# Performance work log

Hardware: AMD Instinct MI355X
Metric: run time of the kernel (lower is better)

The kernel has to match this reference:

```python
import jax, jax.numpy as jnp
import numpy as np

TEMPERATURE = 0.5
EPS = 1e-8  # matches torch cosine_similarity eps guard semantics (norm clamp)


def setup_inputs() -> dict:
    key = jax.random.key(0)
    k1, k2 = jax.random.split(key)
    B, D = 4096, 256
    z_i = jax.random.normal(k1, (B, D), dtype=jnp.float32)
    z_j = jax.random.normal(k2, (B, D), dtype=jnp.float32)
    return {"z_i": z_i, "z_j": z_j}


def reference(z_i, z_j):
    B = z_i.shape[0]
    z = jnp.concatenate([z_i, z_j], axis=0)            # [2B, D]
    # cosine similarity: normalize once, then GEMM
    norm = jnp.maximum(jnp.linalg.norm(z, axis=1, keepdims=True), EPS)
    zn = z / norm                                       # [2B, D]
    sim = zn @ zn.T                                     # [2B, 2B]
    # positives: diag(sim, +B) and diag(sim, -B)
    idx = jnp.arange(B)
    sim_ij = sim[idx, idx + B]
    sim_ji = sim[idx + B, idx]
    positives = jnp.concatenate([sim_ij, sim_ji])       # [2B]
    # masked denominator: exclude self-similarity
    mask = 1.0 - jnp.eye(2 * B, dtype=sim.dtype)
    denom = jnp.sum(mask * jnp.exp(sim / TEMPERATURE), axis=1)  # [2B]
    all_losses = -jnp.log(jnp.exp(positives / TEMPERATURE) / denom)
    return jnp.sum(all_losses) / (2 * B)
```

## Files before the change

kernel.cpp:

```cpp
#include <hip/hip_runtime.h>
#include <hip/hip_bf16.h>
#include <cstdint>
#include <cstddef>
#include <math.h>

#define D 256
#define TEMP_INV 2.0f
#define EPS_NORM 1e-8f
#define NTILES 2080
#define GRID 512

typedef __attribute__((ext_vector_type(8))) short bf16x8;
typedef __attribute__((ext_vector_type(4))) float f32x4;

__global__ void __launch_bounds__(256) normalize_rows(
    const float* __restrict__ zi, const float* __restrict__ zj,
    __hip_bfloat16* __restrict__ zn, float* __restrict__ denom, int B) {
  int row = blockIdx.x * 4 + (threadIdx.x >> 6);
  int lane = threadIdx.x & 63;
  if (threadIdx.x < 4) denom[blockIdx.x * 4 + threadIdx.x] = 0.0f;
  const float* src = (row < B) ? (zi + (size_t)row * D)
                               : (zj + (size_t)(row - B) * D);
  float4 v = ((const float4*)src)[lane];
  float ss = v.x * v.x + v.y * v.y + v.z * v.z + v.w * v.w;
  for (int off = 32; off; off >>= 1) ss += __shfl_xor(ss, off);
  float rn = 1.0f / fmaxf(sqrtf(ss), EPS_NORM);
  union { ushort4 u; __hip_bfloat16 h[4]; } o;
  o.h[0] = __float2bfloat16(v.x * rn);
  o.h[1] = __float2bfloat16(v.y * rn);
  o.h[2] = __float2bfloat16(v.z * rn);
  o.h[3] = __float2bfloat16(v.w * rn);
  ((ushort4*)zn)[(size_t)row * (D / 4) + lane] = o.u;
}

__device__ __forceinline__ void load_lds_16B(const __hip_bfloat16* g,
                                             __hip_bfloat16* l) {
  __builtin_amdgcn_global_load_lds(
      (const __attribute__((address_space(1))) void*)g,
      (__attribute__((address_space(3))) void*)l, 16, 0, 0);
}

__device__ __forceinline__ void decode_tile(int t, int Nb, int& by, int& bx) {
  float fb = (2.0f * Nb + 1.0f -
              sqrtf((float)((2 * Nb + 1) * (2 * Nb + 1) - 8 * t))) * 0.5f;
  int y = (int)fb;
  while ((y + 1) * Nb - ((y + 1) * y) / 2 <= t) ++y;
  while (y * Nb - (y * (y - 1)) / 2 > t) --y;
  by = y;
  bx = y + (t - (y * Nb - (y * (y - 1)) / 2));
}

__device__ __forceinline__ void stage_tile(
    const __hip_bfloat16* __restrict__ zn,
    __hip_bfloat16* Ash, __hip_bfloat16* Bsh,
    int bm, int bn, int k0, int wrow0, int lane) {
  const int lr4 = lane >> 4;
  const int lc16 = lane & 15;
#pragma unroll
  for (int s = 0; s < 8; ++s) {
    int r = wrow0 + s * 4 + lr4;
    int chunk = lc16 ^ (r & 7);
    const __hip_bfloat16* ga = zn + (size_t)(bm + r) * D + k0 + chunk * 8;
    const __hip_bfloat16* gb = zn + (size_t)(bn + r) * D + k0 + chunk * 8;
    load_lds_16B(ga, &Ash[(wrow0 + s * 4) * 128]);
    load_lds_16B(gb, &Bsh[(wrow0 + s * 4) * 128]);
  }
}

__device__ __forceinline__ void compute_k128(
    const __hip_bfloat16* Ash, const __hip_bfloat16* Bsh,
    f32x4 acc[4][4], int wy, int wx, int frow, int quad) {
  const int f7 = frow & 7;
#pragma unroll
  for (int kk = 0; kk < 4; ++kk) {
    bf16x8 a[4], b[4];
#pragma unroll
    for (int i = 0; i < 4; ++i)
      a[i] = *(const bf16x8*)
          &Ash[(wy * 64 + i * 16 + frow) * 128 + (((kk * 4 + quad) ^ f7)) * 8];
#pragma unroll
    for (int j = 0; j < 4; ++j)
      b[j] = *(const bf16x8*)
          &Bsh[(wx * 64 + j * 16 + frow) * 128 + (((kk * 4 + quad) ^ f7)) * 8];
#pragma unroll
    for (int i = 0; i < 4; ++i)
#pragma unroll
      for (int j = 0; j < 4; ++j)
        acc[i][j] =
            __builtin_amdgcn_mfma_f32_16x16x32_bf16(a[i], b[j], acc[i][j], 0, 0, 0);
  }
}

__global__ void __launch_bounds__(256) ntxent_gemm(
    const __hip_bfloat16* __restrict__ zn,
    float* __restrict__ denom, float* __restrict__ pos, int B) {
  __shared__ __align__(16) __hip_bfloat16 Ash[128 * 128];
  __shared__ __align__(16) __hip_bfloat16 Bsh[128 * 128];

  const int Nb = (2 * B) / 128;
  const int tid = threadIdx.x;
  const int wid = tid >> 6;
  const int lane = tid & 63;
  const int wy = wid >> 1, wx = wid & 1;
  const int wrow0 = wid * 32;
  const int frow = lane & 15;
  const int quad = lane >> 4;
  const int colq = lane & 15;

  int t = blockIdx.x;
  int by, bx;
  decode_tile(t, Nb, by, bx);
  int bm = by * 128, bn = bx * 128;
  stage_tile(zn, Ash, Bsh, bm, bn, 0, wrow0, lane);

  while (true) {
    f32x4 acc[4][4] = {};
    __syncthreads();
    compute_k128(Ash, Bsh, acc, wy, wx, frow, quad);
    __syncthreads();
    stage_tile(zn, Ash, Bsh, bm, bn, 128, wrow0, lane);
    __syncthreads();
    compute_k128(Ash, Bsh, acc, wy, wx, frow, quad);
    __syncthreads();

    int nt = t + GRID;
    bool more = (nt < NTILES);
    int nbm = 0, nbn = 0;
    if (more) {
      int nby, nbx;
      decode_tile(nt, Nb, nby, nbx);
      nbm = nby * 128;
      nbn = nbx * 128;
      stage_tile(zn, Ash, Bsh, nbm, nbn, 0, wrow0, lane);
    }

    const bool isDiag = (bm == bn);
    const bool isPos = (bn == bm + B);
    float cs[4] = {0.0f, 0.0f, 0.0f, 0.0f};
#pragma unroll
    for (int i = 0; i < 4; ++i) {
#pragma unroll
      for (int r = 0; r < 4; ++r) {
        int row = bm + wy * 64 + i * 16 + quad * 4 + r;
        float rs = 0.0f;
#pragma unroll
        for (int j = 0; j < 4; ++j) {
          int col = bn + wx * 64 + j * 16 + colq;
          float v = acc[i][j][r];
          float e = __expf(v * TEMP_INV);
          e = (isDiag && col == row) ? 0.0f : e;
          rs += e;
          cs[j] += e;
          if (isPos && col == row + B) { pos[row] = v; pos[col] = v; }
        }
        rs += __shfl_xor(rs, 1);
        rs += __shfl_xor(rs, 2);
        rs += __shfl_xor(rs, 4);
        rs += __shfl_xor(rs, 8);
        if (colq == 0) atomicAdd(&denom[row], rs);
      }
    }
    if (!isDiag) {
#pragma unroll
      for (int j = 0; j < 4; ++j) {
        float c = cs[j];
        c += __shfl_xor(c, 16);
        c += __shfl_xor(c, 32);
        if (quad == 0) atomicAdd(&denom[bn + wx * 64 + j * 16 + colq], c);
      }
    }
    if (!more) break;
    t = nt;
    bm = nbm;
    bn = nbn;
  }
}

__global__ void __launch_bounds__(1024) finalize(
    const float* __restrict__ denom, const float* __restrict__ pos,
    float* __restrict__ out, int N) {
  __shared__ float red[16];
  const int tid = threadIdx.x;
  float s = 0.0f;
  for (int i = tid; i < N / 4; i += 1024) {
    float4 d = ((const float4*)denom)[i];
    float4 p = ((const float4*)pos)[i];
    s += __logf(d.x) - p.x * TEMP_INV;
    s += __logf(d.y) - p.y * TEMP_INV;
    s += __logf(d.z) - p.z * TEMP_INV;
    s += __logf(d.w) - p.w * TEMP_INV;
  }
  for (int off = 32; off; off >>= 1) s += __shfl_xor(s, off);
  if ((tid & 63) == 0) red[tid >> 6] = s;
  __syncthreads();
  if (tid < 16) {
    s = red[tid];
    s += __shfl_xor(s, 1);
    s += __shfl_xor(s, 2);
    s += __shfl_xor(s, 4);
    s += __shfl_xor(s, 8);
    if (tid == 0) out[0] = s / (float)N;
  }
}

extern "C" void kernel_launch(void* const* d_in, const int* in_sizes, int n_in,
                              void* d_out, int out_size, void* d_ws, size_t ws_size,
                              hipStream_t stream) {
  const float* zi = (const float*)d_in[0];
  const float* zj = (const float*)d_in[1];
  const int B = in_sizes[0] / D;
  const int N = 2 * B;

  __hip_bfloat16* zn = (__hip_bfloat16*)d_ws;
  float* denom = (float*)((char*)d_ws + (size_t)N * D * sizeof(__hip_bfloat16));
  float* pos = denom + N;

  normalize_rows<<<N / 4, 256, 0, stream>>>(zi, zj, zn, denom, B);
  ntxent_gemm<<<GRID, 256, 0, stream>>>(zn, denom, pos, B);
  finalize<<<1, 1024, 0, stream>>>(denom, pos, (float*)d_out, N);
}
```

Measured before the change: 122.8 us.

## Launch one block per tile with K=64 register-prefetched LDS staging

Replaces the persistent 512-block loop with a launch of one block per upper-triangular tile (2080 blocks). The K loop is split into four 64-wide steps. The next step's global loads go into registers while MFMAs run on the current LDS buffer, replacing the direct global-to-LDS loads. LDS per block is halved and launch bounds request 3 waves per SIMD to raise occupancy, at the cost of more block launches and extra VGPR pressure from the prefetch registers.

```diff
diff --git a/kernel.cpp b/kernel.cpp
--- a/kernel.cpp
+++ b/kernel.cpp
@@ -8,7 +8,6 @@
 #define TEMP_INV 2.0f
 #define EPS_NORM 1e-8f
 #define NTILES 2080
-#define GRID 512
 
 typedef __attribute__((ext_vector_type(8))) short bf16x8;
 typedef __attribute__((ext_vector_type(4))) float f32x4;
@@ -33,13 +32,6 @@
   ((ushort4*)zn)[(size_t)row * (D / 4) + lane] = o.u;
 }
 
-__device__ __forceinline__ void load_lds_16B(const __hip_bfloat16* g,
-                                             __hip_bfloat16* l) {
-  __builtin_amdgcn_global_load_lds(
-      (const __attribute__((address_space(1))) void*)g,
-      (__attribute__((address_space(3))) void*)l, 16, 0, 0);
-}
-
 __device__ __forceinline__ void decode_tile(int t, int Nb, int& by, int& bx) {
   float fb = (2.0f * Nb + 1.0f -
               sqrtf((float)((2 * Nb + 1) * (2 * Nb + 1) - 8 * t))) * 0.5f;
@@ -50,129 +42,116 @@
   bx = y + (t - (y * Nb - (y * (y - 1)) / 2));
 }
 
-__device__ __forceinline__ void stage_tile(
-    const __hip_bfloat16* __restrict__ zn,
-    __hip_bfloat16* Ash, __hip_bfloat16* Bsh,
-    int bm, int bn, int k0, int wrow0, int lane) {
-  const int lr4 = lane >> 4;
-  const int lc16 = lane & 15;
-#pragma unroll
-  for (int s = 0; s < 8; ++s) {
-    int r = wrow0 + s * 4 + lr4;
-    int chunk = lc16 ^ (r & 7);
-    const __hip_bfloat16* ga = zn + (size_t)(bm + r) * D + k0 + chunk * 8;
-    const __hip_bfloat16* gb = zn + (size_t)(bn + r) * D + k0 + chunk * 8;
-    load_lds_16B(ga, &Ash[(wrow0 + s * 4) * 128]);
-    load_lds_16B(gb, &Bsh[(wrow0 + s * 4) * 128]);
-  }
-}
-
-__device__ __forceinline__ void compute_k128(
-    const __hip_bfloat16* Ash, const __hip_bfloat16* Bsh,
-    f32x4 acc[4][4], int wy, int wx, int frow, int quad) {
-  const int f7 = frow & 7;
-#pragma unroll
-  for (int kk = 0; kk < 4; ++kk) {
-    bf16x8 a[4], b[4];
-#pragma unroll
-    for (int i = 0; i < 4; ++i)
-      a[i] = *(const bf16x8*)
-          &Ash[(wy * 64 + i * 16 + frow) * 128 + (((kk * 4 + quad) ^ f7)) * 8];
-#pragma unroll
-    for (int j = 0; j < 4; ++j)
-      b[j] = *(const bf16x8*)
-          &Bsh[(wx * 64 + j * 16 + frow) * 128 + (((kk * 4 + quad) ^ f7)) * 8];
-#pragma unroll
-    for (int i = 0; i < 4; ++i)
-#pragma unroll
-      for (int j = 0; j < 4; ++j)
-        acc[i][j] =
-            __builtin_amdgcn_mfma_f32_16x16x32_bf16(a[i], b[j], acc[i][j], 0, 0, 0);
-  }
-}
-
-__global__ void __launch_bounds__(256) ntxent_gemm(
+__global__ void __launch_bounds__(256, 3) ntxent_gemm(
     const __hip_bfloat16* __restrict__ zn,
     float* __restrict__ denom, float* __restrict__ pos, int B) {
-  __shared__ __align__(16) __hip_bfloat16 Ash[128 * 128];
-  __shared__ __align__(16) __hip_bfloat16 Bsh[128 * 128];
+  __shared__ __align__(16) __hip_bfloat16 Ash[128 * 64];
+  __shared__ __align__(16) __hip_bfloat16 Bsh[128 * 64];
 
   const int Nb = (2 * B) / 128;
+  int by, bx;
+  decode_tile(blockIdx.x, Nb, by, bx);
+  const int bm = by * 128;
+  const int bn = bx * 128;
+  const bool isDiag = (by == bx);
+  const bool isPos = (bx == by + B / 128);
+
   const int tid = threadIdx.x;
   const int wid = tid >> 6;
   const int lane = tid & 63;
   const int wy = wid >> 1, wx = wid & 1;
   const int wrow0 = wid * 32;
+
+  const int r8 = lane >> 3;
+  const int c8 = lane & 7;
+
   const int frow = lane & 15;
   const int quad = lane >> 4;
+  const int f7 = frow & 7;
+
+  f32x4 acc[4][4] = {};
+  float4 va[4], vb[4];
+
+#pragma unroll
+  for (int s = 0; s < 4; ++s) {
+    int r = wrow0 + s * 8 + r8;
+    va[s] = *(const float4*)(zn + (size_t)(bm + r) * D + c8 * 8);
+    vb[s] = *(const float4*)(zn + (size_t)(bn + r) * D + c8 * 8);
+  }
+
+#pragma unroll
+  for (int k0i = 0; k0i < 4; ++k0i) {
+    __syncthreads();
+#pragma unroll
+    for (int s = 0; s < 4; ++s) {
+      int r = wrow0 + s * 8 + r8;
+      int swz = c8 ^ (r & 7);
+      *(float4*)&Ash[r * 64 + swz * 8] = va[s];
+      *(float4*)&Bsh[r * 64 + swz * 8] = vb[s];
+    }
+    __syncthreads();
+    if (k0i < 3) {
+      const int k0n = (k0i + 1) * 64;
+#pragma unroll
+      for (int s = 0; s < 4; ++s) {
+        int r = wrow0 + s * 8 + r8;
+        va[s] = *(const float4*)(zn + (size_t)(bm + r) * D + k0n + c8 * 8);
+        vb[s] = *(const float4*)(zn + (size_t)(bn + r) * D + k0n + c8 * 8);
+      }
+    }
+#pragma unroll
+    for (int kk = 0; kk < 2; ++kk) {
+      bf16x8 a[4], b[4];
+#pragma unroll
+      for (int i = 0; i < 4; ++i)
+        a[i] = *(const bf16x8*)
+            &Ash[(wy * 64 + i * 16 + frow) * 64 + ((kk * 4 + quad) ^ f7) * 8];
+#pragma unroll
+      for (int j = 0; j < 4; ++j)
+        b[j] = *(const bf16x8*)
+            &Bsh[(wx * 64 + j * 16 + frow) * 64 + ((kk * 4 + quad) ^ f7) * 8];
+#pragma unroll
+      for (int i = 0; i < 4; ++i)
+#pragma unroll
+        for (int j = 0; j < 4; ++j)
+          acc[i][j] =
+              __builtin_amdgcn_mfma_f32_16x16x32_bf16(a[i], b[j], acc[i][j], 0, 0, 0);
+    }
+  }
+
   const int colq = lane & 15;
-
-  int t = blockIdx.x;
-  int by, bx;
-  decode_tile(t, Nb, by, bx);
-  int bm = by * 128, bn = bx * 128;
-  stage_tile(zn, Ash, Bsh, bm, bn, 0, wrow0, lane);
-
-  while (true) {
-    f32x4 acc[4][4] = {};
-    __syncthreads();
-    compute_k128(Ash, Bsh, acc, wy, wx, frow, quad);
-    __syncthreads();
-    stage_tile(zn, Ash, Bsh, bm, bn, 128, wrow0, lane);
-    __syncthreads();
-    compute_k128(Ash, Bsh, acc, wy, wx, frow, quad);
-    __syncthreads();
-
-    int nt = t + GRID;
-    bool more = (nt < NTILES);
-    int nbm = 0, nbn = 0;
-    if (more) {
-      int nby, nbx;
-      decode_tile(nt, Nb, nby, nbx);
-      nbm = nby * 128;
-      nbn = nbx * 128;
-      stage_tile(zn, Ash, Bsh, nbm, nbn, 0, wrow0, lane);
-    }
-
-    const bool isDiag = (bm == bn);
-    const bool isPos = (bn == bm + B);
-    float cs[4] = {0.0f, 0.0f, 0.0f, 0.0f};
-#pragma unroll
-    for (int i = 0; i < 4; ++i) {
-#pragma unroll
-      for (int r = 0; r < 4; ++r) {
-        int row = bm + wy * 64 + i * 16 + quad * 4 + r;
-        float rs = 0.0f;
-#pragma unroll
-        for (int j = 0; j < 4; ++j) {
-          int col = bn + wx * 64 + j * 16 + colq;
-          float v = acc[i][j][r];
-          float e = __expf(v * TEMP_INV);
-          e = (isDiag && col == row) ? 0.0f : e;
-          rs += e;
-          cs[j] += e;
-          if (isPos && col == row + B) { pos[row] = v; pos[col] = v; }
-        }
-        rs += __shfl_xor(rs, 1);
-        rs += __shfl_xor(rs, 2);
-        rs += __shfl_xor(rs, 4);
-        rs += __shfl_xor(rs, 8);
-        if (colq == 0) atomicAdd(&denom[row], rs);
+  float cs[4] = {0.0f, 0.0f, 0.0f, 0.0f};
+#pragma unroll
+  for (int i = 0; i < 4; ++i) {
+#pragma unroll
+    for (int r = 0; r < 4; ++r) {
+      int row = bm + wy * 64 + i * 16 + quad * 4 + r;
+      float rs = 0.0f;
+#pragma unroll
+      for (int j = 0; j < 4; ++j) {
+        int col = bn + wx * 64 + j * 16 + colq;
+        float v = acc[i][j][r];
+        float e = __expf(v * TEMP_INV);
+        e = (isDiag && col == row) ? 0.0f : e;
+        rs += e;
+        cs[j] += e;
+        if (isPos && col == row + B) { pos[row] = v; pos[col] = v; }
       }
-    }
-    if (!isDiag) {
-#pragma unroll
-      for (int j = 0; j < 4; ++j) {
-        float c = cs[j];
-        c += __shfl_xor(c, 16);
-        c += __shfl_xor(c, 32);
-        if (quad == 0) atomicAdd(&denom[bn + wx * 64 + j * 16 + colq], c);
-      }
-    }
-    if (!more) break;
-    t = nt;
-    bm = nbm;
-    bn = nbn;
+      rs += __shfl_xor(rs, 1);
+      rs += __shfl_xor(rs, 2);
+      rs += __shfl_xor(rs, 4);
+      rs += __shfl_xor(rs, 8);
+      if (colq == 0) atomicAdd(&denom[row], rs);
+    }
+  }
+  if (!isDiag) {
+#pragma unroll
+    for (int j = 0; j < 4; ++j) {
+      float c = cs[j];
+      c += __shfl_xor(c, 16);
+      c += __shfl_xor(c, 32);
+      if (quad == 0) atomicAdd(&denom[bn + wx * 64 + j * 16 + colq], c);
+    }
   }
 }
 
@@ -216,6 +195,6 @@
   float* pos = denom + N;
 
   normalize_rows<<<N / 4, 256, 0, stream>>>(zi, zj, zn, denom, B);
-  ntxent_gemm<<<GRID, 256, 0, stream>>>(zn, denom, pos, B);
+  ntxent_gemm<<<NTILES, 256, 0, stream>>>(zn, denom, pos, B);
   finalize<<<1, 1024, 0, stream>>>(denom, pos, (float*)d_out, N);
 }
```

Result: slower. 164.3 us (+33.8%).
